# Kernel tuning notes

Measured on AMD Instinct MI355X. Metric: run time of the kernel, lower is better.

Reference implementation:

```python
import jax, jax.numpy as jnp
import numpy as np

B, T, D_MODEL, D_HEAD = 4, 2048, 1024, 64

def setup_inputs() -> dict:
    key = jax.random.key(0)
    k1, k2, k3, k4 = jax.random.split(key, 4)
    x = jax.random.normal(k1, (B, T, D_MODEL), dtype=jnp.float32)
    # Linear(d_model, d_head) weights stored as [d_model, d_head] for x @ W
    s = 1.0 / np.sqrt(D_MODEL)
    W_Q = jax.random.normal(k2, (D_MODEL, D_HEAD), dtype=jnp.float32) * s
    W_K = jax.random.normal(k3, (D_MODEL, D_HEAD), dtype=jnp.float32) * s
    W_V = jax.random.normal(k4, (D_MODEL, D_HEAD), dtype=jnp.float32) * s
    return {"x": x, "W_Q": W_Q, "W_K": W_K, "W_V": W_V}

def reference(x, W_Q, W_K, W_V):
    d_head = W_Q.shape[-1]
    Q = jnp.einsum('btm,md->btd', x, W_Q)
    K = jnp.einsum('btm,md->btd', x, W_K)
    V = jnp.einsum('btm,md->btd', x, W_V)
    A = jnp.einsum('bid,bjd->bij', Q, K) / jnp.sqrt(jnp.asarray(d_head, x.dtype))
    T_ = x.shape[1]
    causal = jnp.tril(jnp.ones((T_, T_), dtype=bool))  # [T, T]
    A = jnp.where(causal, A, -jnp.inf)
    A = jax.nn.softmax(A, axis=-1)
    return jnp.einsum('bij,bjd->bid', A, V)
```

## Files before the change

kernel.cpp:

```cpp
#include <hip/hip_runtime.h>
#include <hip/hip_bf16.h>

#define NB 4
#define NT 2048
#define DM 1024
#define DH 64
#define CHUNK3 3
#define SLOTS 6

typedef __attribute__((ext_vector_type(8))) short bf16x8;
typedef __attribute__((ext_vector_type(4))) float f32x4;
typedef unsigned short u16;
typedef unsigned int u32;

static __device__ __forceinline__ u16 f2b(float f) {
    __hip_bfloat16 h = __float2bfloat16(f);
    return __builtin_bit_cast(u16, h);
}
static __device__ __forceinline__ float b2f(u16 h) {
    return __builtin_bit_cast(float, (u32)h << 16);
}
static __device__ __forceinline__ void gld16(const void* g, void* l) {
    __builtin_amdgcn_global_load_lds((const __attribute__((address_space(1))) void*)g,
                                     (__attribute__((address_space(3))) void*)l, 16, 0, 0);
}
#define BAR() __builtin_amdgcn_s_barrier()
#define SBAR() __builtin_amdgcn_sched_barrier(0)

__global__ __launch_bounds__(256) void wt_conv(
    const float* __restrict__ WQ, const float* __restrict__ WK,
    const float* __restrict__ WV, u16* __restrict__ wt)
{
    __shared__ u16 tl[64][68];
    const int which = blockIdx.y, kt = blockIdx.x;
    const float* W = (which == 0) ? WQ : (which == 1) ? WK : WV;
    #pragma unroll
    for (int i = 0; i < 4; ++i) {
        int r = (threadIdx.x >> 4) + i * 16;
        int c = (threadIdx.x & 15) * 4;
        float4 v = *(const float4*)&W[(size_t)(kt * 64 + r) * DH + c];
        tl[r][c] = f2b(v.x); tl[r][c + 1] = f2b(v.y);
        tl[r][c + 2] = f2b(v.z); tl[r][c + 3] = f2b(v.w);
    }
    __syncthreads();
    int d = threadIdx.x >> 2, kc = (threadIdx.x & 3) * 16;
    u16 buf[16];
    #pragma unroll
    for (int j = 0; j < 16; ++j) buf[j] = tl[kc + j][d];
    u16* dst = wt + which * 65536 + d * 1024 + kt * 64 + kc;
    *(uint4*)dst = *(uint4*)&buf[0];
    *(uint4*)(dst + 8) = *(uint4*)&buf[8];
}

__global__ __launch_bounds__(256) void qkv_gemm(
    const float* __restrict__ x, const u16* __restrict__ wt,
    u16* __restrict__ Qb, u16* __restrict__ Kb, u16* __restrict__ Vt)
{
    __shared__ u16 xbuf[3][4096];
    __shared__ u16 wsm[3][4096];
    const int tid = threadIdx.x, lane = tid & 63, w = tid >> 6;
    const int l15 = lane & 15, g = lane >> 4;
    const int row0 = blockIdx.x * 64;
    const int which = blockIdx.y;
    const u16* Wg = wt + which * 65536;

    const int xr_ = tid >> 2, xc4 = tid & 3;
    const float* xsrc = x + (size_t)(row0 + xr_) * DM + xc4 * 16;
    const u32 xsw = (u32)((xr_ & 7) << 4);
    const u32 xa0 = (u32)(xr_ * 128 + xc4 * 32) ^ xsw;
    const u32 xa1 = (u32)(xr_ * 128 + xc4 * 32 + 16) ^ xsw;

    f32x4 xv[4];
    auto xload = [&](int kt) {
        const float* p = xsrc + kt * 64;
        xv[0] = *(const f32x4*)(p);
        xv[1] = *(const f32x4*)(p + 4);
        xv[2] = *(const f32x4*)(p + 8);
        xv[3] = *(const f32x4*)(p + 12);
    };
    auto stageW = [&](int kt, int bi) {
        #pragma unroll
        for (int i = 0; i < 2; ++i) {
            u32 D = (u32)(w * 2048 + i * 1024 + lane * 16);
            u32 r = D >> 7, c = D & 127;
            u32 cs = c ^ ((r & 7) << 4);
            gld16(Wg + (size_t)r * 1024 + kt * 64 + (cs >> 1),
                  (char*)&wsm[bi][0] + w * 2048 + i * 1024);
        }
    };

    f32x4 acc[4];
    #pragma unroll
    for (int i = 0; i < 4; ++i) acc[i] = {0.f, 0.f, 0.f, 0.f};

    xload(0);
    stageW(0, 0);
    const int arow = w * 16 + l15;
    const u32 asw = (u32)((arow & 7) << 4);

    #pragma unroll
    for (int kt = 0; kt < 16; ++kt) {
        const int cur = kt % 3;
        asm volatile("s_waitcnt vmcnt(2)" ::: "memory");
        {
            u16 tmp[16];
            #pragma unroll
            for (int i = 0; i < 4; ++i)
                #pragma unroll
                for (int j = 0; j < 4; ++j) tmp[i * 4 + j] = f2b(xv[i][j]);
            *(uint4*)((char*)&xbuf[cur][0] + xa0) = *(uint4*)&tmp[0];
            *(uint4*)((char*)&xbuf[cur][0] + xa1) = *(uint4*)&tmp[8];
        }
        if (kt < 15) {
            xload(kt + 1);
            stageW(kt + 1, (kt + 1) % 3);
            asm volatile("s_waitcnt vmcnt(6)" ::: "memory");
        } else {
            asm volatile("s_waitcnt vmcnt(0)" ::: "memory");
        }
        asm volatile("s_waitcnt lgkmcnt(0)" ::: "memory");
        BAR();
        SBAR();
        const char* xb = (const char*)&xbuf[cur][0];
        const char* wb = (const char*)&wsm[cur][0];
        #pragma unroll
        for (int ks = 0; ks < 2; ++ks) {
            bf16x8 afrag = *(const bf16x8*)(xb + ((u32)(arow * 128 + ks * 64 + g * 16) ^ asw));
            __builtin_amdgcn_s_setprio(1);
            #pragma unroll
            for (int nt = 0; nt < 4; ++nt) {
                int brow = nt * 16 + l15;
                u32 bb = (u32)(brow * 128 + ks * 64 + g * 16);
                bf16x8 bfrag = *(const bf16x8*)(wb + (bb ^ ((brow & 7) << 4)));
                acc[nt] = __builtin_amdgcn_mfma_f32_16x16x32_bf16(afrag, bfrag, acc[nt], 0, 0, 0);
            }
            __builtin_amdgcn_s_setprio(0);
        }
    }
    #pragma unroll
    for (int nt = 0; nt < 4; ++nt) {
        int dcol = nt * 16 + l15;
        #pragma unroll
        for (int r = 0; r < 4; ++r) {
            int row = row0 + w * 16 + g * 4 + r;
            float v = acc[nt][r];
            if (which == 0)      Qb[(size_t)row * DH + dcol] = f2b(v * 0.125f);
            else if (which == 1) Kb[(size_t)row * DH + dcol] = f2b(v);
            else { int bb2 = row >> 11, t = row & 2047;
                   Vt[(size_t)bb2 * DH * NT + (size_t)dcol * NT + t] = f2b(v); }
        }
    }
}

__global__ __launch_bounds__(256) void attn(
    const u16* __restrict__ Qb, const u16* __restrict__ Kb,
    const u16* __restrict__ Vt, u16* __restrict__ pOt, float* __restrict__ pml)
{
    __shared__ u16 k_lds[2][8192];
    __shared__ u16 v_lds[2][8192];
    __shared__ f32x4 p_lds[4][256];

    const int tid = threadIdx.x, lane = tid & 63, w = tid >> 6;
    const int l15 = lane & 15, g = lane >> 4;
    const int b = blockIdx.y;

    int flat = blockIdx.x, qb = 0, nc, nt128;
    for (;;) {
        nt128 = (qb + 2) >> 1;
        nc = (nt128 + CHUNK3 - 1) / CHUNK3;
        if (flat < nc) break;
        flat -= nc; ++qb;
    }
    const int chunk = flat;
    const int t0 = chunk * CHUNK3;
    const int t1 = min(t0 + CHUNK3, nt128);
    const int tD = nt128 - 1;
    const int delta = qb * 64 - tD * 128;
    const int q0 = qb * 64;

    const u16* Qg = Qb + ((size_t)b * NT + q0 + w * 16) * DH;
    const u16* Kg = Kb + (size_t)b * NT * DH;
    const u16* Vg = Vt + (size_t)b * DH * NT;

    auto stage = [&](int t, int bi) {
        const int j0 = t * 128;
        #pragma unroll
        for (int i = 0; i < 4; ++i) {
            u32 D = (u32)(w * 4096 + i * 1024 + lane * 16);
            {
                u32 r = D >> 7, c = D & 127;
                u32 cs = c ^ ((r & 7) << 4);
                gld16(Kg + (size_t)(j0 + r) * DH + (cs >> 1),
                      (char*)&k_lds[bi][0] + w * 4096 + i * 1024);
            }
            {
                u32 r = D >> 8, c = D & 255;
                u32 cs = c ^ ((r & 15) << 4);
                gld16(Vg + (size_t)r * NT + j0 + (cs >> 1),
                      (char*)&v_lds[bi][0] + w * 4096 + i * 1024);
            }
        }
    };
    stage(t0, 0);

    bf16x8 qf[2];
    qf[0] = *(const bf16x8*)(Qg + l15 * DH + g * 8);
    qf[1] = *(const bf16x8*)(Qg + l15 * DH + 32 + g * 8);

    float m_run = -INFINITY, l_run = 0.f;
    f32x4 oacc[4];
    #pragma unroll
    for (int nt = 0; nt < 4; ++nt) oacc[nt] = {0.f, 0.f, 0.f, 0.f};

    char* pw = (char*)&p_lds[w][0];
    const u32 pswz = (u32)((l15 & 15) << 4);
    const int q_local = w * 16 + l15;

    for (int t = t0; t < t1; ++t) {
        const int cur = (t - t0) & 1;
        if (t + 1 < t1) {
            stage(t + 1, cur ^ 1);
            asm volatile("s_waitcnt vmcnt(8)" ::: "memory");
        } else {
            asm volatile("s_waitcnt vmcnt(0)" ::: "memory");
        }
        BAR();
        SBAR();
        const char* kb = (const char*)&k_lds[cur][0];
        const char* vb = (const char*)&v_lds[cur][0];

        f32x4 sacc[8];
        #pragma unroll
        for (int f = 0; f < 8; ++f) sacc[f] = {0.f, 0.f, 0.f, 0.f};
        __builtin_amdgcn_s_setprio(1);
        #pragma unroll
        for (int ks = 0; ks < 2; ++ks) {
            #pragma unroll
            for (int f = 0; f < 8; ++f) {
                int arow = f * 16 + l15;
                u32 aa = (u32)(arow * 128 + ks * 64 + g * 16);
                bf16x8 kf = *(const bf16x8*)(kb + (aa ^ ((arow & 7) << 4)));
                sacc[f] = __builtin_amdgcn_mfma_f32_16x16x32_bf16(kf, qf[ks], sacc[f], 0, 0, 0);
            }
        }
        __builtin_amdgcn_s_setprio(0);
        if (t == tD) {
            #pragma unroll
            for (int f = 0; f < 8; ++f)
                #pragma unroll
                for (int r = 0; r < 4; ++r)
                    if (f * 16 + g * 4 + r > delta + q_local) sacc[f][r] = -1e30f;
        }
        float mx = -INFINITY;
        #pragma unroll
        for (int f = 0; f < 8; ++f) {
            float a = fmaxf(fmaxf(sacc[f][0], sacc[f][1]),
                            fmaxf(sacc[f][2], sacc[f][3]));
            mx = fmaxf(mx, a);
        }
        mx = fmaxf(mx, __shfl_xor(mx, 16));
        mx = fmaxf(mx, __shfl_xor(mx, 32));
        const float m_new = fmaxf(m_run, mx);
        const float alpha = __expf(m_run - m_new);
        float p[8][4];
        float ps = 0.f;
        #pragma unroll
        for (int f = 0; f < 8; ++f)
            #pragma unroll
            for (int r = 0; r < 4; ++r) {
                float pv = __expf(sacc[f][r] - m_new);
                p[f][r] = pv; ps += pv;
            }
        ps += __shfl_xor(ps, 16);
        ps += __shfl_xor(ps, 32);
        l_run = l_run * alpha + ps;
        m_run = m_new;
        #pragma unroll
        for (int nt = 0; nt < 4; ++nt)
            #pragma unroll
            for (int r = 0; r < 4; ++r) oacc[nt][r] *= alpha;

        #pragma unroll
        for (int f = 0; f < 8; ++f) {
            uint2 pk;
            pk.x = (u32)f2b(p[f][0]) | ((u32)f2b(p[f][1]) << 16);
            pk.y = (u32)f2b(p[f][2]) | ((u32)f2b(p[f][3]) << 16);
            u32 a = (u32)(l15 * 256 + f * 32 + g * 8) ^ pswz;
            *(uint2*)(pw + a) = pk;
        }
        bf16x8 pb_[4];
        #pragma unroll
        for (int ksj = 0; ksj < 4; ++ksj)
            pb_[ksj] = *(const bf16x8*)(pw + ((u32)(l15 * 256 + ksj * 64 + g * 16) ^ pswz));

        __builtin_amdgcn_s_setprio(1);
        #pragma unroll
        for (int ksj = 0; ksj < 4; ++ksj) {
            #pragma unroll
            for (int nt = 0; nt < 4; ++nt) {
                int arow = nt * 16 + l15;
                u32 aa = (u32)(arow * 256 + ksj * 64 + g * 16);
                bf16x8 vf = *(const bf16x8*)(vb + (aa ^ ((arow & 15) << 4)));
                oacc[nt] = __builtin_amdgcn_mfma_f32_16x16x32_bf16(vf, pb_[ksj], oacc[nt], 0, 0, 0);
            }
        }
        __builtin_amdgcn_s_setprio(0);
        BAR();
    }

    const int slot = (b * 32 + qb) * SLOTS + chunk;
    u16* Op = pOt + (size_t)slot * 4096;
    #pragma unroll
    for (int nt = 0; nt < 4; ++nt)
        #pragma unroll
        for (int r = 0; r < 4; ++r)
            Op[(nt * 16 + g * 4 + r) * 64 + w * 16 + l15] = f2b(oacc[nt][r]);
    if (g == 0) {
        float* mlp = pml + (size_t)slot * 128;
        mlp[(w * 16 + l15) * 2]     = m_run;
        mlp[(w * 16 + l15) * 2 + 1] = l_run;
    }
}

__global__ __launch_bounds__(256) void merge(
    const u16* __restrict__ pOt, const float* __restrict__ pml,
    float* __restrict__ out)
{
    __shared__ float tl[64][65];
    const int bq = blockIdx.x;
    const int b = bq >> 5, qb = bq & 31;
    const int nt128 = (qb + 2) >> 1;
    const int nc = (nt128 + CHUNK3 - 1) / CHUNK3;
    const int base = bq * SLOTS;
    const int q = threadIdx.x & 63, ds = threadIdx.x >> 6;

    float m = -INFINITY;
    for (int c = 0; c < nc; ++c)
        m = fmaxf(m, pml[(size_t)(base + c) * 128 + q * 2]);
    float lsum = 0.f;
    float acc[16];
    #pragma unroll
    for (int i = 0; i < 16; ++i) acc[i] = 0.f;
    for (int c = 0; c < nc; ++c) {
        const float mc = pml[(size_t)(base + c) * 128 + q * 2];
        const float lc = pml[(size_t)(base + c) * 128 + q * 2 + 1];
        const float wc = __expf(mc - m);
        lsum += wc * lc;
        const u16* Op = pOt + (size_t)(base + c) * 4096;
        #pragma unroll
        for (int i = 0; i < 16; ++i)
            acc[i] += wc * b2f(Op[(ds * 16 + i) * 64 + q]);
    }
    const float inv = 1.f / lsum;
    #pragma unroll
    for (int i = 0; i < 16; ++i) tl[q][ds * 16 + i] = acc[i] * inv;
    __syncthreads();
    const int q2 = threadIdx.x >> 2, dc = threadIdx.x & 3;
    float* orow = out + ((size_t)b * NT + qb * 64 + q2) * 64 + dc * 16;
    #pragma unroll
    for (int j4 = 0; j4 < 4; ++j4) {
        float4 v = { tl[q2][dc * 16 + j4 * 4 + 0], tl[q2][dc * 16 + j4 * 4 + 1],
                     tl[q2][dc * 16 + j4 * 4 + 2], tl[q2][dc * 16 + j4 * 4 + 3] };
        *(float4*)&orow[j4 * 4] = v;
    }
}

extern "C" void kernel_launch(void* const* d_in, const int* in_sizes, int n_in,
                              void* d_out, int out_size, void* d_ws, size_t ws_size,
                              hipStream_t stream) {
    const float* x  = (const float*)d_in[0];
    const float* WQ = (const float*)d_in[1];
    const float* WK = (const float*)d_in[2];
    const float* WV = (const float*)d_in[3];
    float* out = (float*)d_out;

    char* ws = (char*)d_ws;
    u16*   Qb  = (u16*)ws;
    u16*   Kb  = (u16*)(ws + 1048576);
    u16*   Vt  = (u16*)(ws + 2097152);
    u16*   Wt  = (u16*)(ws + 3145728);
    u16*   pOt = (u16*)(ws + 3538944);
    float* pml = (float*)(ws + 3538944 + 6291456);

    wt_conv<<<dim3(16, 3), 256, 0, stream>>>(WQ, WK, WV, Wt);
    qkv_gemm<<<dim3(128, 3), 256, 0, stream>>>(x, Wt, Qb, Kb, Vt);
    attn<<<dim3(102, NB), 256, 0, stream>>>(Qb, Kb, Vt, pOt, pml);
    merge<<<NB * 32, 256, 0, stream>>>(pOt, pml, out);
}
```

Before: 40.94 us.

## Remove split-KV chunking and merge kernel; attention writes final output directly

Each attention block now processes the full causal key range for one 64-row query block and normalises and writes fp32 output itself. This eliminates the separate merge kernel launch and the bf16 partial output and m/l traffic. In exchange, only 128 blocks launch and their work varies greatly, with the longest block doing many more sequential key tiles, which risks poor CU utilisation and load imbalance.

```diff
diff --git a/kernel.cpp b/kernel.cpp
--- a/kernel.cpp
+++ b/kernel.cpp
@@ -5,8 +5,6 @@
 #define NT 2048
 #define DM 1024
 #define DH 64
-#define CHUNK3 3
-#define SLOTS 6
 
 typedef __attribute__((ext_vector_type(8))) short bf16x8;
 typedef __attribute__((ext_vector_type(4))) float f32x4;
@@ -16,9 +14,6 @@
 static __device__ __forceinline__ u16 f2b(float f) {
     __hip_bfloat16 h = __float2bfloat16(f);
     return __builtin_bit_cast(u16, h);
-}
-static __device__ __forceinline__ float b2f(u16 h) {
-    return __builtin_bit_cast(float, (u32)h << 16);
 }
 static __device__ __forceinline__ void gld16(const void* g, void* l) {
     __builtin_amdgcn_global_load_lds((const __attribute__((address_space(1))) void*)g,
@@ -154,26 +149,18 @@
 
 __global__ __launch_bounds__(256) void attn(
     const u16* __restrict__ Qb, const u16* __restrict__ Kb,
-    const u16* __restrict__ Vt, u16* __restrict__ pOt, float* __restrict__ pml)
+    const u16* __restrict__ Vt, float* __restrict__ out)
 {
-    __shared__ u16 k_lds[2][8192];
-    __shared__ u16 v_lds[2][8192];
-    __shared__ f32x4 p_lds[4][256];
+    __shared__ __align__(16) char smem[81920];
+    u16 (*k_lds)[8192] = (u16(*)[8192])(smem);
+    u16 (*v_lds)[8192] = (u16(*)[8192])(smem + 32768);
+    f32x4* p_lds = (f32x4*)(smem + 65536);
 
     const int tid = threadIdx.x, lane = tid & 63, w = tid >> 6;
     const int l15 = lane & 15, g = lane >> 4;
     const int b = blockIdx.y;
-
-    int flat = blockIdx.x, qb = 0, nc, nt128;
-    for (;;) {
-        nt128 = (qb + 2) >> 1;
-        nc = (nt128 + CHUNK3 - 1) / CHUNK3;
-        if (flat < nc) break;
-        flat -= nc; ++qb;
-    }
-    const int chunk = flat;
-    const int t0 = chunk * CHUNK3;
-    const int t1 = min(t0 + CHUNK3, nt128);
+    const int qb = blockIdx.x;
+    const int nt128 = (qb + 2) >> 1;
     const int tD = nt128 - 1;
     const int delta = qb * 64 - tD * 128;
     const int q0 = qb * 64;
@@ -201,7 +188,7 @@
             }
         }
     };
-    stage(t0, 0);
+    stage(0, 0);
 
     bf16x8 qf[2];
     qf[0] = *(const bf16x8*)(Qg + l15 * DH + g * 8);
@@ -212,13 +199,13 @@
     #pragma unroll
     for (int nt = 0; nt < 4; ++nt) oacc[nt] = {0.f, 0.f, 0.f, 0.f};
 
-    char* pw = (char*)&p_lds[w][0];
+    char* pw = (char*)&p_lds[w * 256];
     const u32 pswz = (u32)((l15 & 15) << 4);
     const int q_local = w * 16 + l15;
 
-    for (int t = t0; t < t1; ++t) {
-        const int cur = (t - t0) & 1;
-        if (t + 1 < t1) {
+    for (int t = 0; t < nt128; ++t) {
+        const int cur = t & 1;
+        if (t + 1 < nt128) {
             stage(t + 1, cur ^ 1);
             asm volatile("s_waitcnt vmcnt(8)" ::: "memory");
         } else {
@@ -308,59 +295,20 @@
         BAR();
     }
 
-    const int slot = (b * 32 + qb) * SLOTS + chunk;
-    u16* Op = pOt + (size_t)slot * 4096;
+    const float inv = 1.f / l_run;
+    float (*ol)[68] = (float(*)[68])(void*)smem;
     #pragma unroll
     for (int nt = 0; nt < 4; ++nt)
         #pragma unroll
         for (int r = 0; r < 4; ++r)
-            Op[(nt * 16 + g * 4 + r) * 64 + w * 16 + l15] = f2b(oacc[nt][r]);
-    if (g == 0) {
-        float* mlp = pml + (size_t)slot * 128;
-        mlp[(w * 16 + l15) * 2]     = m_run;
-        mlp[(w * 16 + l15) * 2 + 1] = l_run;
-    }
-}
-
-__global__ __launch_bounds__(256) void merge(
-    const u16* __restrict__ pOt, const float* __restrict__ pml,
-    float* __restrict__ out)
-{
-    __shared__ float tl[64][65];
-    const int bq = blockIdx.x;
-    const int b = bq >> 5, qb = bq & 31;
-    const int nt128 = (qb + 2) >> 1;
-    const int nc = (nt128 + CHUNK3 - 1) / CHUNK3;
-    const int base = bq * SLOTS;
-    const int q = threadIdx.x & 63, ds = threadIdx.x >> 6;
-
-    float m = -INFINITY;
-    for (int c = 0; c < nc; ++c)
-        m = fmaxf(m, pml[(size_t)(base + c) * 128 + q * 2]);
-    float lsum = 0.f;
-    float acc[16];
-    #pragma unroll
-    for (int i = 0; i < 16; ++i) acc[i] = 0.f;
-    for (int c = 0; c < nc; ++c) {
-        const float mc = pml[(size_t)(base + c) * 128 + q * 2];
-        const float lc = pml[(size_t)(base + c) * 128 + q * 2 + 1];
-        const float wc = __expf(mc - m);
-        lsum += wc * lc;
-        const u16* Op = pOt + (size_t)(base + c) * 4096;
-        #pragma unroll
-        for (int i = 0; i < 16; ++i)
-            acc[i] += wc * b2f(Op[(ds * 16 + i) * 64 + q]);
-    }
-    const float inv = 1.f / lsum;
-    #pragma unroll
-    for (int i = 0; i < 16; ++i) tl[q][ds * 16 + i] = acc[i] * inv;
+            ol[nt * 16 + g * 4 + r][w * 16 + l15] = oacc[nt][r] * inv;
     __syncthreads();
-    const int q2 = threadIdx.x >> 2, dc = threadIdx.x & 3;
-    float* orow = out + ((size_t)b * NT + qb * 64 + q2) * 64 + dc * 16;
+    const int q2 = tid >> 2, dc = tid & 3;
+    float* orow = out + ((size_t)b * NT + q0 + q2) * 64 + dc * 16;
     #pragma unroll
     for (int j4 = 0; j4 < 4; ++j4) {
-        float4 v = { tl[q2][dc * 16 + j4 * 4 + 0], tl[q2][dc * 16 + j4 * 4 + 1],
-                     tl[q2][dc * 16 + j4 * 4 + 2], tl[q2][dc * 16 + j4 * 4 + 3] };
+        float4 v = { ol[dc * 16 + j4 * 4 + 0][q2], ol[dc * 16 + j4 * 4 + 1][q2],
+                     ol[dc * 16 + j4 * 4 + 2][q2], ol[dc * 16 + j4 * 4 + 3][q2] };
         *(float4*)&orow[j4 * 4] = v;
     }
 }
@@ -375,15 +323,12 @@
     float* out = (float*)d_out;
 
     char* ws = (char*)d_ws;
-    u16*   Qb  = (u16*)ws;
-    u16*   Kb  = (u16*)(ws + 1048576);
-    u16*   Vt  = (u16*)(ws + 2097152);
-    u16*   Wt  = (u16*)(ws + 3145728);
-    u16*   pOt = (u16*)(ws + 3538944);
-    float* pml = (float*)(ws + 3538944 + 6291456);
+    u16* Qb = (u16*)ws;
+    u16* Kb = (u16*)(ws + 1048576);
+    u16* Vt = (u16*)(ws + 2097152);
+    u16* Wt = (u16*)(ws + 3145728);
 
     wt_conv<<<dim3(16, 3), 256, 0, stream>>>(WQ, WK, WV, Wt);
     qkv_gemm<<<dim3(128, 3), 256, 0, stream>>>(x, Wt, Qb, Kb, Vt);
-    attn<<<dim3(102, NB), 256, 0, stream>>>(Qb, Kb, Vt, pOt, pml);
-    merge<<<NB * 32, 256, 0, stream>>>(pOt, pml, out);
-}
+    attn<<<dim3(32, NB), 256, 0, stream>>>(Qb, Kb, Vt, out);
+}
```

New measurement: 52.91 us. 29.2% more time.
